# Kernel optimization log

Hardware: AMD Instinct MI355X
Metric: run time of the kernel (lower is better)

Reference implementation:

```python
import jax, jax.numpy as jnp
import numpy as np

B, D = 64, 1024
TAU = 1.0
NEG_SLOPE = 0.01  # torch LeakyReLU default


def setup_inputs() -> dict:
    key = jax.random.key(0)
    ks = jax.random.split(key, 7)
    lim = 1.0 / np.sqrt(D)
    return {
        "x": jax.random.normal(ks[0], (B, D), dtype=jnp.float32),
        "W1": jax.random.uniform(ks[1], (D, D), jnp.float32, -lim, lim),
        "b1": jax.random.uniform(ks[2], (D,), jnp.float32, -lim, lim),
        "W2": jax.random.uniform(ks[3], (D, D), jnp.float32, -lim, lim),
        "b2": jax.random.uniform(ks[4], (D,), jnp.float32, -lim, lim),
        "W3": jax.random.uniform(ks[5], (2, D), jnp.float32, -lim, lim),
        "b3": jax.random.uniform(ks[6], (2,), jnp.float32, -lim, lim),
    }


def _leaky(h):
    return jnp.where(h >= 0, h, NEG_SLOPE * h)


def _neural_sort(scores):
    # scores: [B, D]
    d = scores.shape[1]
    s = scores[..., None]                                  # [B, D, 1]
    A = jnp.abs(s - jnp.swapaxes(s, 1, 2))                 # [B, D, D] pairwise |s_i - s_j|
    # A @ (ones @ ones^T) == row-sum of A broadcast over columns
    Bsum = jnp.sum(A, axis=-1, keepdims=True)              # [B, D, 1]
    scaling = (d - 1 - 2 * jnp.arange(d)).astype(scores.dtype)  # (d+1-2*(i+1))
    C = s * scaling[None, None, :]                         # [B, D, D]
    P_max = jnp.swapaxes(C - Bsum, 1, 2)                   # [B, D, D]
    return jax.nn.softmax(P_max / TAU, axis=-1)


def reference(x, W1, b1, W2, b2, W3, b3):
    P_hat = _neural_sort(x)                                # [B, D, D]
    xs = jnp.einsum("bij,bj->bi", P_hat, x)                # soft-sorted x
    h = _leaky(xs @ W1.T + b1)
    h = _leaky(h @ W2.T + b2)
    return h @ W3.T + b3                                   # [B, 2]
```

## Files before the change

kernel.cpp:

```cpp
#include <hip/hip_runtime.h>
#include <math.h>

constexpr int Bn = 64;
constexpr int Dn = 1024;
constexpr int NBK = 128;
constexpr float LOG2E = 1.4426950408889634f;
constexpr float LN2   = 0.6931471805599453f;

__device__ __forceinline__ float exp2_fast(float v) {
#if defined(__has_builtin)
#if __has_builtin(__builtin_amdgcn_exp2f)
  return __builtin_amdgcn_exp2f(v);
#else
  return exp2f(v);
#endif
#else
  return exp2f(v);
#endif
}

__global__ __launch_bounds__(512) void k_sortsoft(
    const float* __restrict__ x, float* __restrict__ xs_out,
    float* __restrict__ out) {
  __shared__ float  xs_[Dn];
  __shared__ float2 prs_[Dn];
  __shared__ int    bkt_[Dn];
  __shared__ float4 desc_[128];
  __shared__ int   cnt[NBK], base_[NBK], off_[NBK];
  __shared__ float Ssum[NBK], cN[NBK], cS[NBK];
  __shared__ float redM[8][64], redE[8][64], redD[8][64];

  int b   = blockIdx.x >> 4;
  int rc  = blockIdx.x & 15;
  int tid = threadIdx.x;

  if (tid < NBK) { cnt[tid] = 0; off_[tid] = 0; Ssum[tid] = 0.f; }
  if (blockIdx.x == 0 && tid < 128) out[tid] = 0.f;
  __syncthreads();

  float2 v2 = *(const float2*)(x + b * Dn + tid * 2);
  float xv[2] = {v2.x, v2.y};
  int bk[2];
#pragma unroll
  for (int u = 0; u < 2; ++u) {
    float z = exp2_fast(-2.455532f * xv[u]);
    float p = 1.f / (1.f + z);
    int t = (int)(p * 128.f);
    bk[u] = t < 0 ? 0 : (t > 127 ? 127 : t);
    atomicAdd(&cnt[bk[u]], 1);
    atomicAdd(&Ssum[bk[u]], xv[u]);
  }
  __syncthreads();

  if (tid < 64) {
    int c0 = cnt[tid], c1 = cnt[tid + 64];
    float f0 = Ssum[tid], f1 = Ssum[tid + 64];
    int s0 = c0, s1 = c1;
    float g0 = f0, g1 = f1;
#pragma unroll
    for (int d = 1; d < 64; d <<= 1) {
      int o0 = __shfl_up(s0, d, 64), o1 = __shfl_up(s1, d, 64);
      float h0 = __shfl_up(g0, d, 64), h1 = __shfl_up(g1, d, 64);
      if (tid >= d) { s0 += o0; s1 += o1; g0 += h0; g1 += h1; }
    }
    int   T0 = __shfl(s0, 63, 64);
    float G0 = __shfl(g0, 63, 64);
    float G1 = __shfl(g1, 63, 64);
    float Stot = G0 + G1;
    int nlo0 = s0 - c0;
    base_[tid] = nlo0;
    cN[tid] = (float)(2 * nlo0 + c0 - Dn);
    float slo0 = g0 - f0;
    cS[tid] = Stot - 2.f * slo0 - f0;
    int nlo1 = T0 + s1 - c1;
    base_[tid + 64] = nlo1;
    cN[tid + 64] = (float)(2 * nlo1 + c1 - Dn);
    float slo1 = G0 + g1 - f1;
    cS[tid + 64] = Stot - 2.f * slo1 - f1;
  }
  __syncthreads();

#pragma unroll
  for (int u = 0; u < 2; ++u) {
    int pos = base_[bk[u]] + atomicAdd(&off_[bk[u]], 1);
    xs_[pos] = xv[u];
    bkt_[pos] = bk[u];
  }
  __syncthreads();

#pragma unroll
  for (int r = 0; r < 2; ++r) {
    int p = r * 512 + tid;
    float xp = xs_[p];
    int q = bkt_[p];
    int lo = base_[q], hi = lo + cnt[q];
    float local = 0.f;
    for (int k = lo; k < hi; ++k) local += fabsf(xp - xs_[k]);
    float Bs = fmaf(xp, cN[q], cS[q]) + local;
    prs_[p] = make_float2(xp * LOG2E, -Bs * LOG2E);
  }
  __syncthreads();

  if (tid < 128) {
    int base = tid * 8;
    float xlo = xs_[base], xhi = xlo;
    int ilo = base, ihi = base;
#pragma unroll
    for (int k = 1; k < 8; ++k) {
      float xx = xs_[base + k];
      if (xx < xlo) { xlo = xx; ilo = base + k; }
      if (xx > xhi) { xhi = xx; ihi = base + k; }
    }
    float2 plo = prs_[ilo], phi = prs_[ihi];
    desc_[tid] = make_float4(plo.x, plo.y, phi.x, phi.y);
  }
  __syncthreads();

  int w = tid >> 6, lane = tid & 63;
  int i = rc * 64 + lane;
  float sc = (float)(Dn - 1 - 2 * i);
  float gm[16];
  float m = -3.4e38f;
#pragma unroll 8
  for (int q = 0; q < 16; ++q) {
    float4 d = desc_[q * 8 + w];
    float t0 = fmaf(sc, d.x, d.y);
    float t1 = fmaf(sc, d.z, d.w);
    float g = fmaxf(t0, t1);
    gm[q] = g;
    m = fmaxf(m, g);
  }
  redM[w][lane] = m;
  __syncthreads();
  float M = fmaxf(fmaxf(fmaxf(redM[0][lane], redM[1][lane]),
                        fmaxf(redM[2][lane], redM[3][lane])),
                  fmaxf(fmaxf(redM[4][lane], redM[5][lane]),
                        fmaxf(redM[6][lane], redM[7][lane])));
  float thresh = M - 32.f;

  float se = 0.f, sd = 0.f;
#pragma unroll 4
  for (int q = 0; q < 16; ++q) {
    if (__any(gm[q] > thresh)) {
      int base = (q * 8 + w) * 8;
#pragma unroll
      for (int u = 0; u < 8; ++u) {
        float2 v = prs_[base + u];
        float e = exp2_fast(fmaf(sc, v.x, v.y - M));
        se += e;
        sd = fmaf(e, v.x, sd);
      }
    }
  }
  redE[w][lane] = se;
  redD[w][lane] = sd;
  __syncthreads();
  if (tid < 64) {
    float SE = ((redE[0][lane] + redE[1][lane]) + (redE[2][lane] + redE[3][lane])) +
               ((redE[4][lane] + redE[5][lane]) + (redE[6][lane] + redE[7][lane]));
    float SD = ((redD[0][lane] + redD[1][lane]) + (redD[2][lane] + redD[3][lane])) +
               ((redD[4][lane] + redD[5][lane]) + (redD[6][lane] + redD[7][lane]));
    xs_out[b * Dn + rc * 64 + lane] = SD / SE * LN2;
  }
}

template <bool TAIL>
__global__ __launch_bounds__(256) void layer_kernel(
    const float* __restrict__ in, const float* __restrict__ W,
    const float* __restrict__ bias, float* __restrict__ out,
    const float* __restrict__ W3, const float* __restrict__ b3,
    float* __restrict__ out2) {
  __shared__ float s[8 * Dn];
  __shared__ float rk[4][32];
  __shared__ float r2[8][8][2];
  int xcd = blockIdx.x & 7;
  int idx = blockIdx.x >> 3;
  int nc = xcd * 16 + (idx & 15);
  int bc = idx >> 4;
  int tid = threadIdx.x;
  const float* src = in + bc * 8 * Dn;
#pragma unroll
  for (int u = 0; u < 8; ++u) {
    int gl = u * 256 + tid;
    int r = gl >> 8, g = gl & 255;
    int gs = g ^ ((g >> 3) & 7);
    *(float4*)&s[r * Dn + gs * 4] = *(const float4*)(src + gl * 4);
  }
  __syncthreads();

  int w = tid >> 6, lane = tid & 63;
  int cq = w & 1, kh = w >> 1;
  int n0 = nc * 8 + cq * 4;
  const float* wp = W + (size_t)n0 * Dn + kh * 512 + lane * 8;
  float acc[32];
#pragma unroll
  for (int i = 0; i < 32; ++i) acc[i] = 0.f;
#pragma unroll
  for (int j = 0; j < 2; ++j) {
    float4 wv0 = *(const float4*)(wp + 0 * Dn + j * 4);
    float4 wv1 = *(const float4*)(wp + 1 * Dn + j * 4);
    float4 wv2 = *(const float4*)(wp + 2 * Dn + j * 4);
    float4 wv3 = *(const float4*)(wp + 3 * Dn + j * 4);
    int g = kh * 128 + lane * 2 + j;
    int gs = g ^ ((g >> 3) & 7);
    const float* sp = s + gs * 4;
#pragma unroll
    for (int bl = 0; bl < 8; ++bl) {
      float4 av = *(const float4*)(sp + bl * Dn);
      acc[bl * 4 + 0] = fmaf(av.x, wv0.x, fmaf(av.y, wv0.y,
                        fmaf(av.z, wv0.z, fmaf(av.w, wv0.w, acc[bl * 4 + 0]))));
      acc[bl * 4 + 1] = fmaf(av.x, wv1.x, fmaf(av.y, wv1.y,
                        fmaf(av.z, wv1.z, fmaf(av.w, wv1.w, acc[bl * 4 + 1]))));
      acc[bl * 4 + 2] = fmaf(av.x, wv2.x, fmaf(av.y, wv2.y,
                        fmaf(av.z, wv2.z, fmaf(av.w, wv2.w, acc[bl * 4 + 2]))));
      acc[bl * 4 + 3] = fmaf(av.x, wv3.x, fmaf(av.y, wv3.y,
                        fmaf(av.z, wv3.z, fmaf(av.w, wv3.w, acc[bl * 4 + 3]))));
    }
  }

#pragma unroll
  for (int bit = 0; bit < 5; ++bit) {
    int d = 1 << bit;
    bool hi = (lane & d) != 0;
#pragma unroll
    for (int i = 0; i < (16 >> bit); ++i) {
      float keep = hi ? acc[2 * i + 1] : acc[2 * i];
      float send = hi ? acc[2 * i] : acc[2 * i + 1];
      acc[i] = keep + __shfl_xor(send, d, 64);
    }
  }
  float t = acc[0];
  t += __shfl_xor(t, 32, 64);
  if (lane < 32) rk[w][lane] = t;
  __syncthreads();

  if (tid < 64) {
    int bl2 = tid >> 3, col = tid & 7;
    int cq2 = col >> 2, cl2 = col & 3;
    int o = bl2 * 4 + cl2;
    int n2 = nc * 8 + col;
    float hs = rk[cq2][o] + rk[cq2 + 2][o];
    float h = hs + bias[n2];
    h = h >= 0.f ? h : 0.01f * h;
    if (!TAIL) {
      out[(bc * 8 + bl2) * Dn + n2] = h;
    } else {
      r2[bl2][col][0] = h * W3[n2];
      r2[bl2][col][1] = h * W3[Dn + n2];
    }
  }
  if (TAIL) {
    __syncthreads();
    if (tid < 16) {
      int bl2 = tid >> 1, o = tid & 1;
      float tt = 0.f;
#pragma unroll
      for (int q = 0; q < 8; ++q) tt += r2[bl2][q][o];
      if (nc == 0) tt += b3[o];
      atomicAdd(out2 + (bc * 8 + bl2) * 2 + o, tt);
    }
  }
}

extern "C" void kernel_launch(void* const* d_in, const int* in_sizes, int n_in,
                              void* d_out, int out_size, void* d_ws, size_t ws_size,
                              hipStream_t stream) {
  const float* x  = (const float*)d_in[0];
  const float* W1 = (const float*)d_in[1];
  const float* b1 = (const float*)d_in[2];
  const float* W2 = (const float*)d_in[3];
  const float* b2 = (const float*)d_in[4];
  const float* W3 = (const float*)d_in[5];
  const float* b3 = (const float*)d_in[6];
  float* out = (float*)d_out;
  float* ws = (float*)d_ws;

  float* xs = ws;
  float* h1 = xs + Bn * Dn;

  k_sortsoft<<<Bn * 16, 512, 0, stream>>>(x, xs, out);
  layer_kernel<false><<<1024, 256, 0, stream>>>(xs, W1, b1, h1,
                                                nullptr, nullptr, nullptr);
  layer_kernel<true><<<1024, 256, 0, stream>>>(h1, W2, b2, nullptr,
                                               W3, b3, out);
}
```

Baseline: 98.95 us.

## Split sort prologue into per-batch kernel to stop redundant recompute across row chunks

The sorting and pairwise-sum prologue used to run in each of the 16 row-chunk blocks per batch. It now runs once per batch in a separate 1024-thread kernel that writes the per-element pairs and bucket descriptors to global workspace. The softmax kernel then only loads those values. This removes 16x redundant prologue work, at the cost of an extra kernel launch and a global round trip for about 8 KB per batch.

```diff
diff --git a/kernel.cpp b/kernel.cpp
--- a/kernel.cpp
+++ b/kernel.cpp
@@ -19,36 +19,31 @@
 #endif
 }
 
-__global__ __launch_bounds__(512) void k_sortsoft(
-    const float* __restrict__ x, float* __restrict__ xs_out,
-    float* __restrict__ out) {
+__global__ __launch_bounds__(1024) void k_sort(
+    const float* __restrict__ x, float2* __restrict__ prs_g,
+    float4* __restrict__ desc_g, float* __restrict__ out) {
   __shared__ float  xs_[Dn];
   __shared__ float2 prs_[Dn];
   __shared__ int    bkt_[Dn];
-  __shared__ float4 desc_[128];
   __shared__ int   cnt[NBK], base_[NBK], off_[NBK];
   __shared__ float Ssum[NBK], cN[NBK], cS[NBK];
-  __shared__ float redM[8][64], redE[8][64], redD[8][64];
-
-  int b   = blockIdx.x >> 4;
-  int rc  = blockIdx.x & 15;
+
+  int b   = blockIdx.x;
   int tid = threadIdx.x;
 
   if (tid < NBK) { cnt[tid] = 0; off_[tid] = 0; Ssum[tid] = 0.f; }
-  if (blockIdx.x == 0 && tid < 128) out[tid] = 0.f;
-  __syncthreads();
-
-  float2 v2 = *(const float2*)(x + b * Dn + tid * 2);
-  float xv[2] = {v2.x, v2.y};
-  int bk[2];
-#pragma unroll
-  for (int u = 0; u < 2; ++u) {
-    float z = exp2_fast(-2.455532f * xv[u]);
+  if (b == 0 && tid < 128) out[tid] = 0.f;
+  __syncthreads();
+
+  float xv = x[b * Dn + tid];
+  int bk;
+  {
+    float z = exp2_fast(-2.455532f * xv);
     float p = 1.f / (1.f + z);
     int t = (int)(p * 128.f);
-    bk[u] = t < 0 ? 0 : (t > 127 ? 127 : t);
-    atomicAdd(&cnt[bk[u]], 1);
-    atomicAdd(&Ssum[bk[u]], xv[u]);
+    bk = t < 0 ? 0 : (t > 127 ? 127 : t);
+    atomicAdd(&cnt[bk], 1);
+    atomicAdd(&Ssum[bk], xv);
   }
   __syncthreads();
 
@@ -80,24 +75,23 @@
   }
   __syncthreads();
 
-#pragma unroll
-  for (int u = 0; u < 2; ++u) {
-    int pos = base_[bk[u]] + atomicAdd(&off_[bk[u]], 1);
-    xs_[pos] = xv[u];
-    bkt_[pos] = bk[u];
-  }
-  __syncthreads();
-
-#pragma unroll
-  for (int r = 0; r < 2; ++r) {
-    int p = r * 512 + tid;
-    float xp = xs_[p];
-    int q = bkt_[p];
+  {
+    int pos = base_[bk] + atomicAdd(&off_[bk], 1);
+    xs_[pos] = xv;
+    bkt_[pos] = bk;
+  }
+  __syncthreads();
+
+  {
+    float xp = xs_[tid];
+    int q = bkt_[tid];
     int lo = base_[q], hi = lo + cnt[q];
     float local = 0.f;
     for (int k = lo; k < hi; ++k) local += fabsf(xp - xs_[k]);
     float Bs = fmaf(xp, cN[q], cS[q]) + local;
-    prs_[p] = make_float2(xp * LOG2E, -Bs * LOG2E);
+    float2 pr = make_float2(xp * LOG2E, -Bs * LOG2E);
+    prs_[tid] = pr;
+    prs_g[(size_t)b * Dn + tid] = pr;
   }
   __syncthreads();
 
@@ -112,8 +106,23 @@
       if (xx > xhi) { xhi = xx; ihi = base + k; }
     }
     float2 plo = prs_[ilo], phi = prs_[ihi];
-    desc_[tid] = make_float4(plo.x, plo.y, phi.x, phi.y);
-  }
+    desc_g[b * 128 + tid] = make_float4(plo.x, plo.y, phi.x, phi.y);
+  }
+}
+
+__global__ __launch_bounds__(512) void k_soft(
+    const float2* __restrict__ prs_g, const float4* __restrict__ desc_g,
+    float* __restrict__ xs_out) {
+  __shared__ __align__(16) float2 prs_[Dn];
+  __shared__ float4 desc_[128];
+  __shared__ float redM[8][64], redE[8][64], redD[8][64];
+
+  int b   = blockIdx.x >> 4;
+  int rc  = blockIdx.x & 15;
+  int tid = threadIdx.x;
+
+  ((float4*)prs_)[tid] = ((const float4*)(prs_g + (size_t)b * Dn))[tid];
+  if (tid < 128) desc_[tid] = desc_g[b * 128 + tid];
   __syncthreads();
 
   int w = tid >> 6, lane = tid & 63;
@@ -275,10 +284,13 @@
   float* out = (float*)d_out;
   float* ws = (float*)d_ws;
 
-  float* xs = ws;
-  float* h1 = xs + Bn * Dn;
-
-  k_sortsoft<<<Bn * 16, 512, 0, stream>>>(x, xs, out);
+  float*  xs     = ws;
+  float*  h1     = xs + Bn * Dn;
+  float2* prs_g  = (float2*)(h1 + Bn * Dn);
+  float4* desc_g = (float4*)(prs_g + Bn * Dn);
+
+  k_sort<<<Bn, 1024, 0, stream>>>(x, prs_g, desc_g, out);
+  k_soft<<<Bn * 16, 512, 0, stream>>>(prs_g, desc_g, xs);
   layer_kernel<false><<<1024, 256, 0, stream>>>(xs, W1, b1, h1,
                                                 nullptr, nullptr, nullptr);
   layer_kernel<true><<<1024, 256, 0, stream>>>(h1, W2, b2, nullptr,
```

Measured after the change: 95.24 us. -3.7%, faster.
